# Kernel optimization log

Measured on AMD Instinct MI355X. Metric: run time of the kernel, lower is better.

## Reference

```python
import jax, jax.numpy as jnp
import numpy as np

N_NODES = 100000
N_EDGES = 1600000
N_GRAPHS = 2000
F_IN = 64
HID = 64


def setup_inputs() -> dict:
    key = jax.random.key(0)
    ks = jax.random.split(key, 8)
    h = jax.random.normal(ks[0], (N_NODES, F_IN), jnp.float32)
    edge_src = jax.random.randint(ks[1], (N_EDGES,), 0, N_NODES, jnp.int32)
    edge_dst = jax.random.randint(ks[2], (N_EDGES,), 0, N_NODES, jnp.int32)
    graph_ids = jnp.sort(jax.random.randint(ks[3], (N_NODES,), 0, N_GRAPHS, jnp.int32))
    # GraphConv weights (glorot-ish scale) and biases, 3 layers 64->64
    sc = 1.0 / np.sqrt(F_IN)
    W0 = jax.random.normal(ks[4], (F_IN, HID), jnp.float32) * sc
    W1 = jax.random.normal(ks[5], (HID, HID), jnp.float32) * sc
    W2 = jax.random.normal(ks[6], (HID, HID), jnp.float32) * sc
    b0 = jnp.zeros((HID,), jnp.float32)
    b1 = jnp.zeros((HID,), jnp.float32)
    b2 = jnp.zeros((HID,), jnp.float32)
    return dict(h=h, edge_src=edge_src, edge_dst=edge_dst, graph_ids=graph_ids,
                W0=W0, b0=b0, W1=W1, b1=b1, W2=W2, b2=b2)


def _gcn_layer(h, W, b, src, dst, out_deg_isqrt, in_deg_isqrt, apply_relu):
    # DGL GraphConv, norm='both': D_in^{-1/2} A D_out^{-1/2} h W + b
    hw = (h * out_deg_isqrt[:, None]) @ W          # weight/norm commute with sum
    m = jax.ops.segment_sum(hw[src], dst, num_segments=N_NODES)  # gather->scatter-add
    m = m * in_deg_isqrt[:, None] + b
    return jax.nn.relu(m) if apply_relu else m


def reference(h, edge_src, edge_dst, graph_ids, W0, b0, W1, b1, W2, b2):
    ones = jnp.ones((N_EDGES,), h.dtype)
    out_deg = jnp.clip(jax.ops.segment_sum(ones, edge_src, num_segments=N_NODES), 1.0, None)
    in_deg = jnp.clip(jax.ops.segment_sum(ones, edge_dst, num_segments=N_NODES), 1.0, None)
    odi = jax.lax.rsqrt(out_deg)
    idi = jax.lax.rsqrt(in_deg)
    params = [(W0, b0), (W1, b1), (W2, b2)]
    for i, (W, b) in enumerate(params):
        h = _gcn_layer(h, W, b, edge_src, edge_dst, odi, idi, apply_relu=(i < len(params) - 1))
    # self.factor = sqrt(dim) / mean(||h||) computed as python float -> detached constant
    factor = jnp.sqrt(jnp.asarray(HID, h.dtype)) / jnp.mean(jnp.linalg.norm(h, axis=1))
    factor = jax.lax.stop_gradient(factor)
    h = h * factor
    # SumPooling over batched graphs
    return jax.ops.segment_sum(h, graph_ids, num_segments=N_GRAPHS)
```

## Files before the change

kernel.cpp:

```cpp
#include <hip/hip_runtime.h>
#include <hip/hip_fp16.h>

#define N_NODES 100000
#define N_EDGES 1600000
#define N_GRAPHS 2000
#define HID 64
#define NB 391
#define CAP 5120
#define NSUP 16
#define SUPW 6400
#define CAP_S 106496
#define CH_A 2048
#define NCH_A ((N_EDGES + CH_A - 1) / CH_A)
#define BCH 4096
#define NCHB 26
#define GATHER_GRID 2048
#define GEMM_GRID 512
#define N_GROUPS (N_NODES / 4)
#define N_TILE16 (N_NODES / 16)

typedef _Float16 half8 __attribute__((ext_vector_type(8)));
typedef float f32x4 __attribute__((ext_vector_type(4)));

__global__ __launch_bounds__(256) void k_zero_i32(int* __restrict__ p, int n) {
    int i = blockIdx.x * 256 + threadIdx.x;
    if (i < n) p[i] = 0;
}

__global__ __launch_bounds__(256) void k_passA(const int* __restrict__ src, const int* __restrict__ dst,
                                               int* __restrict__ scur_dst, int* __restrict__ scur_src,
                                               unsigned* __restrict__ sup_dst,
                                               unsigned short* __restrict__ sup_src) {
    __shared__ unsigned stD[CH_A];
    __shared__ unsigned short stS[CH_A];
    __shared__ unsigned char binD[CH_A];
    __shared__ unsigned char binS[CH_A];
    __shared__ int lcntD[NSUP], lexD[NSUP], lofD[NSUP], runD[NSUP];
    __shared__ int lcntS[NSUP], lexS[NSUP], lofS[NSUP], runS[NSUP];
    int tid = threadIdx.x;
    int e0 = blockIdx.x * CH_A;
    int n = min(CH_A, N_EDGES - e0);
    if (tid < NSUP) { lcntD[tid] = 0; lcntS[tid] = 0; }
    __syncthreads();
    int sv[8], dv[8];
#pragma unroll
    for (int k = 0; k < 8; ++k) {
        int i = k * 256 + tid;
        if (i < n) { sv[k] = src[e0 + i]; dv[k] = dst[e0 + i]; }
        else dv[k] = -1;
    }
#pragma unroll
    for (int k = 0; k < 8; ++k)
        if (dv[k] >= 0) {
            atomicAdd(&lcntD[dv[k] / SUPW], 1);
            atomicAdd(&lcntS[sv[k] / SUPW], 1);
        }
    __syncthreads();
    if (tid == 0)  { int a = 0; for (int i = 0; i < NSUP; ++i) { lexD[i] = a; lofD[i] = a; a += lcntD[i]; } }
    if (tid == 64) { int a = 0; for (int i = 0; i < NSUP; ++i) { lexS[i] = a; lofS[i] = a; a += lcntS[i]; } }
    __syncthreads();
#pragma unroll
    for (int k = 0; k < 8; ++k)
        if (dv[k] >= 0) {
            int d = dv[k], s = sv[k];
            int bD = d / SUPW;
            int pD = atomicAdd(&lofD[bD], 1);
            stD[pD] = ((unsigned)(d - bD * SUPW) << 17) | (unsigned)s;
            binD[pD] = (unsigned char)bD;
            int bS = s / SUPW;
            int pS = atomicAdd(&lofS[bS], 1);
            stS[pS] = (unsigned short)(s - bS * SUPW);
            binS[pS] = (unsigned char)bS;
        }
    __syncthreads();
    if (tid < NSUP) runD[tid] = lcntD[tid] ? atomicAdd(&scur_dst[tid], lcntD[tid]) : 0;
    if (tid >= 128 && tid < 128 + NSUP) {
        int b = tid - 128;
        runS[b] = lcntS[b] ? atomicAdd(&scur_src[b], lcntS[b]) : 0;
    }
    __syncthreads();
    for (int i = tid; i < n; i += 256) {
        int b = binD[i];
        int pos = runD[b] + (i - lexD[b]);
        if (pos < CAP_S) sup_dst[(size_t)b * CAP_S + pos] = stD[i];
    }
    for (int i = tid; i < n; i += 256) {
        int b = binS[i];
        int pos = runS[b] + (i - lexS[b]);
        if (pos < CAP_S) sup_src[(size_t)b * CAP_S + pos] = stS[i];
    }
}

__global__ __launch_bounds__(256) void k_passB(const unsigned* __restrict__ sup_dst,
                                               const unsigned short* __restrict__ sup_src,
                                               const int* __restrict__ scur_dst,
                                               const int* __restrict__ scur_src,
                                               int* __restrict__ gcur_dst, int* __restrict__ gcur_src,
                                               unsigned* __restrict__ part_dst,
                                               unsigned char* __restrict__ part_src) {
    __shared__ unsigned st[BCH];
    __shared__ unsigned char bin[BCH];
    __shared__ int lcnt[25], lex[25], lof[25], run[25];
    int tid = threadIdx.x;
    int isSrc = blockIdx.x >= NSUP * NCHB;
    int bx = isSrc ? blockIdx.x - NSUP * NCHB : blockIdx.x;
    int sb = bx / NCHB, ch = bx % NCHB;
    int total = isSrc ? scur_src[sb] : scur_dst[sb];
    total = min(total, CAP_S);
    int o0 = ch * BCH;
    int n = min(BCH, total - o0);
    if (n <= 0) return;
    int bg0 = sb * 25;
    if (tid < 25) lcnt[tid] = 0;
    __syncthreads();

    if (!isSrc) {
        unsigned ev[16];
        int bb[16];
#pragma unroll
        for (int k = 0; k < 16; ++k) {
            int i = k * 256 + tid;
            if (i < n) {
                unsigned e = sup_dst[(size_t)sb * CAP_S + o0 + i];
                ev[k] = e;
                bb[k] = (int)(e >> 25);
                atomicAdd(&lcnt[bb[k]], 1);
            } else bb[k] = -1;
        }
        __syncthreads();
        if (tid == 0) { int a = 0; for (int i = 0; i < 25; ++i) { lex[i] = a; lof[i] = a; a += lcnt[i]; } }
        __syncthreads();
#pragma unroll
        for (int k = 0; k < 16; ++k)
            if (bb[k] >= 0) {
                unsigned e = ev[k];
                unsigned s = e & 0x1FFFFu;
                unsigned low = (e >> 17) & 255u;
                int p = atomicAdd(&lof[bb[k]], 1);
                st[p] = (s << 8) | low;
                bin[p] = (unsigned char)bb[k];
            }
        __syncthreads();
        if (tid < 25) run[tid] = lcnt[tid] ? atomicAdd(&gcur_dst[bg0 + tid], lcnt[tid]) : 0;
        __syncthreads();
        for (int i = tid; i < n; i += 256) {
            int b = bin[i];
            int pos = run[b] + (i - lex[b]);
            if (pos < CAP) part_dst[(size_t)(bg0 + b) * CAP + pos] = st[i];
        }
    } else {
        unsigned char* st8 = (unsigned char*)st;
        int rv[16];
        int bb[16];
#pragma unroll
        for (int k = 0; k < 16; ++k) {
            int i = k * 256 + tid;
            if (i < n) {
                int r = (int)sup_src[(size_t)sb * CAP_S + o0 + i];
                rv[k] = r;
                bb[k] = r >> 8;
                atomicAdd(&lcnt[bb[k]], 1);
            } else bb[k] = -1;
        }
        __syncthreads();
        if (tid == 0) { int a = 0; for (int i = 0; i < 25; ++i) { lex[i] = a; lof[i] = a; a += lcnt[i]; } }
        __syncthreads();
#pragma unroll
        for (int k = 0; k < 16; ++k)
            if (bb[k] >= 0) {
                int p = atomicAdd(&lof[bb[k]], 1);
                st8[p] = (unsigned char)(rv[k] & 255);
                bin[p] = (unsigned char)bb[k];
            }
        __syncthreads();
        if (tid < 25) run[tid] = lcnt[tid] ? atomicAdd(&gcur_src[bg0 + tid], lcnt[tid]) : 0;
        __syncthreads();
        for (int i = tid; i < n; i += 256) {
            int b = bin[i];
            int pos = run[b] + (i - lex[b]);
            if (pos < CAP) part_src[(size_t)(bg0 + b) * CAP + pos] = st8[i];
        }
    }
}

__global__ __launch_bounds__(256) void k_csr_count(const unsigned* __restrict__ part_dst,
                                                   const unsigned char* __restrict__ part_src,
                                                   const int* __restrict__ gcur_dst,
                                                   const int* __restrict__ gcur_src,
                                                   int* __restrict__ rowbeg, int* __restrict__ rowend,
                                                   float* __restrict__ idi, float* __restrict__ odi,
                                                   int* __restrict__ col) {
    __shared__ int cnt[256];
    __shared__ int cur[256];
    __shared__ int wsum[4];
    int tid = threadIdx.x;
    if (blockIdx.x >= NB) {
        int b = blockIdx.x - NB;
        int nE = min(gcur_src[b], CAP);
        const unsigned char* pb = part_src + (size_t)b * CAP;
        cnt[tid] = 0;
        __syncthreads();
        for (int i = tid; i < nE; i += 256) atomicAdd(&cnt[pb[i]], 1);
        __syncthreads();
        int v = b * 256 + tid;
        if (v < N_NODES) odi[v] = rsqrtf((float)max(cnt[tid], 1));
        return;
    }
    int b = blockIdx.x;
    int base = b * CAP;
    int nE = min(gcur_dst[b], CAP);
    const unsigned* pb = part_dst + (size_t)b * CAP;
    cnt[tid] = 0;
    __syncthreads();
    for (int i = tid; i < nE; i += 256) atomicAdd(&cnt[pb[i] & 255], 1);
    __syncthreads();
    int c = cnt[tid];
    int incl = c;
#pragma unroll
    for (int off = 1; off < 64; off <<= 1) {
        int t = __shfl_up(incl, off, 64);
        if ((tid & 63) >= off) incl += t;
    }
    if ((tid & 63) == 63) wsum[tid >> 6] = incl;
    __syncthreads();
    int add = 0;
    for (int w = 0; w < (tid >> 6); ++w) add += wsum[w];
    incl += add;
    int excl = incl - c;
    int v = b * 256 + tid;
    if (v < N_NODES) {
        rowbeg[v] = base + excl;
        rowend[v] = base + incl;
        idi[v] = rsqrtf((float)max(c, 1));
    }
    cur[tid] = excl;
    __syncthreads();
    for (int i = tid; i < nE; i += 256) {
        unsigned e = pb[i];
        int p = atomicAdd(&cur[e & 255], 1);
        col[base + p] = (int)(e >> 8);
    }
}

template <int F32IN>
__global__ __launch_bounds__(256) void k_gemm_mfma(const void* __restrict__ inv,
                                                   const float* __restrict__ W,
                                                   const float* __restrict__ odi,
                                                   __half* __restrict__ zs) {
    __shared__ _Float16 Wt[64 * 64];
    int tid = threadIdx.x;
    for (int i = tid; i < 4096; i += 256) {
        int k = i >> 6, j = i & 63;
        Wt[j * 64 + k] = (_Float16)W[i];
    }
    __syncthreads();

    int lane = tid & 63;
    int wid = tid >> 6;
    int lrow = lane & 15;
    int lgrp = lane >> 4;

    half8 Bf[4][2];
#pragma unroll
    for (int nt = 0; nt < 4; ++nt)
#pragma unroll
        for (int kh = 0; kh < 2; ++kh)
            Bf[nt][kh] = *(half8*)&Wt[(nt * 16 + lrow) * 64 + kh * 32 + lgrp * 8];

    for (int t = blockIdx.x * 4 + wid; t < N_TILE16; t += GEMM_GRID * 4) {
        int v0 = t * 16;
        half8 a0, a1;
        if (F32IN) {
            const float* A = (const float*)inv + (size_t)(v0 + lrow) * 64 + lgrp * 8;
            float4 f0 = *(const float4*)A;
            float4 f1 = *(const float4*)(A + 4);
            float4 g0 = *(const float4*)(A + 32);
            float4 g1 = *(const float4*)(A + 36);
            a0[0] = (_Float16)f0.x; a0[1] = (_Float16)f0.y; a0[2] = (_Float16)f0.z; a0[3] = (_Float16)f0.w;
            a0[4] = (_Float16)f1.x; a0[5] = (_Float16)f1.y; a0[6] = (_Float16)f1.z; a0[7] = (_Float16)f1.w;
            a1[0] = (_Float16)g0.x; a1[1] = (_Float16)g0.y; a1[2] = (_Float16)g0.z; a1[3] = (_Float16)g0.w;
            a1[4] = (_Float16)g1.x; a1[5] = (_Float16)g1.y; a1[6] = (_Float16)g1.z; a1[7] = (_Float16)g1.w;
        } else {
            const _Float16* A = (const _Float16*)inv + (size_t)(v0 + lrow) * 64 + lgrp * 8;
            a0 = *(const half8*)A;
            a1 = *(const half8*)(A + 32);
        }
        f32x4 acc[4];
#pragma unroll
        for (int nt = 0; nt < 4; ++nt) { acc[nt] = (f32x4)0.f; }
#pragma unroll
        for (int nt = 0; nt < 4; ++nt) {
            acc[nt] = __builtin_amdgcn_mfma_f32_16x16x32_f16(a0, Bf[nt][0], acc[nt], 0, 0, 0);
            acc[nt] = __builtin_amdgcn_mfma_f32_16x16x32_f16(a1, Bf[nt][1], acc[nt], 0, 0, 0);
        }
#pragma unroll
        for (int r = 0; r < 4; ++r) {
            int node = v0 + lgrp * 4 + r;
            float w = odi[node];
#pragma unroll
            for (int nt = 0; nt < 4; ++nt)
                zs[(size_t)node * 64 + nt * 16 + lrow] = __float2half_rn(acc[nt][r] * w);
        }
    }
}

template <int RELU, int LAST>
__global__ __launch_bounds__(256) void k_gather(const __half* __restrict__ zs, const int* __restrict__ rowbeg,
                                                const int* __restrict__ rowend, const int* __restrict__ col,
                                                const float* __restrict__ idi, const float* __restrict__ b,
                                                __half* __restrict__ xout, float* __restrict__ outF,
                                                float* __restrict__ partials) {
    __shared__ float part[4];
    int tid = threadIdx.x;
    int lane = tid & 63;
    int wid = tid >> 6;
    int half = lane >> 5;
    int fp = lane & 31;
    float2 bias2 = *(const float2*)&b[fp * 2];
    float nacc = 0.f;

    for (int g = blockIdx.x; g < N_GROUPS; g += GATHER_GRID) {
        int v = __builtin_amdgcn_readfirstlane(g * 4 + wid);
        int beg = rowbeg[v], end = rowend[v];
        float2 a0 = {0.f, 0.f}, a1 = {0.f, 0.f}, a2 = {0.f, 0.f}, a3 = {0.f, 0.f};
        int p = beg;
        for (; p + 16 <= end; p += 16) {
#pragma unroll
            for (int j = 0; j < 8; ++j) {
                int s = col[p + 2 * j + half];
                float2 f = __half22float2(*((const __half2*)(zs + (size_t)s * 64) + fp));
                if ((j & 3) == 0) { a0.x += f.x; a0.y += f.y; }
                else if ((j & 3) == 1) { a1.x += f.x; a1.y += f.y; }
                else if ((j & 3) == 2) { a2.x += f.x; a2.y += f.y; }
                else { a3.x += f.x; a3.y += f.y; }
            }
        }
        if (p + 8 <= end) {
#pragma unroll
            for (int j = 0; j < 4; ++j) {
                int s = col[p + 2 * j + half];
                float2 f = __half22float2(*((const __half2*)(zs + (size_t)s * 64) + fp));
                if (j == 0) { a0.x += f.x; a0.y += f.y; }
                else if (j == 1) { a1.x += f.x; a1.y += f.y; }
                else if (j == 2) { a2.x += f.x; a2.y += f.y; }
                else { a3.x += f.x; a3.y += f.y; }
            }
            p += 8;
        }
        if (p < end) {
#pragma unroll
            for (int j = 0; j < 4; ++j) {
                int e = p + 2 * j + half;
                int q = (e < end) ? e : (end - 1);
                int s = col[q];
                float2 f = __half22float2(*((const __half2*)(zs + (size_t)s * 64) + fp));
                float m = (e < end) ? 1.f : 0.f;
                if (j == 0) { a0.x = fmaf(f.x, m, a0.x); a0.y = fmaf(f.y, m, a0.y); }
                else if (j == 1) { a1.x = fmaf(f.x, m, a1.x); a1.y = fmaf(f.y, m, a1.y); }
                else if (j == 2) { a2.x = fmaf(f.x, m, a2.x); a2.y = fmaf(f.y, m, a2.y); }
                else { a3.x = fmaf(f.x, m, a3.x); a3.y = fmaf(f.y, m, a3.y); }
            }
        }
        float2 a;
        a.x = (a0.x + a1.x) + (a2.x + a3.x);
        a.y = (a0.y + a1.y) + (a2.y + a3.y);
        a.x += __shfl_xor(a.x, 32, 64);
        a.y += __shfl_xor(a.y, 32, 64);
        float iv = idi[v];
        float2 o;
        o.x = fmaf(a.x, iv, bias2.x);
        o.y = fmaf(a.y, iv, bias2.y);
        if (RELU) { o.x = fmaxf(o.x, 0.f); o.y = fmaxf(o.y, 0.f); }

        if (LAST) {
            if (half == 0) *(float2*)&outF[(size_t)v * 64 + fp * 2] = o;
            float s = o.x * o.x + o.y * o.y;
#pragma unroll
            for (int off = 32; off > 0; off >>= 1) s += __shfl_xor(s, off, 64);
            if (lane == 0) nacc += sqrtf(0.5f * s);
        } else {
            if (half == 0)
                *((__half2*)(xout + (size_t)v * 64) + fp) = __floats2half2_rn(o.x, o.y);
        }
    }

    if (LAST) {
        if (lane == 0) part[wid] = nacc;
        __syncthreads();
        if (tid == 0) partials[blockIdx.x] = part[0] + part[1] + part[2] + part[3];
    }
}

__global__ __launch_bounds__(256) void k_reduce_factor(const float* __restrict__ partials,
                                                       float* __restrict__ factor) {
    __shared__ float sd[256];
    int tid = threadIdx.x;
    float s = 0.f;
    for (int i = tid; i < GATHER_GRID; i += 256) s += partials[i];
    sd[tid] = s;
    __syncthreads();
    for (int off = 128; off > 0; off >>= 1) {
        if (tid < off) sd[tid] += sd[tid + off];
        __syncthreads();
    }
    if (tid == 0) factor[0] = 8.0f * (float)N_NODES / sd[0];
}

#define POOL_CHUNK 32
__global__ __launch_bounds__(256) void k_pool(const float* __restrict__ h, const int* __restrict__ gid,
                                              const float* __restrict__ factor, float* __restrict__ out) {
    int wave = (blockIdx.x * 256 + threadIdx.x) >> 6;
    int lane = threadIdx.x & 63;
    int v0 = wave * POOL_CHUNK;
    if (v0 >= N_NODES) return;
    float f = factor[0];
    int vend = min(v0 + POOL_CHUNK, N_NODES);
    int gprev = gid[v0];
    float acc = 0.f;
    for (int v = v0; v < vend; ++v) {
        int g = gid[v];
        if (g != gprev) {
            atomicAdd(&out[(size_t)gprev * 64 + lane], acc);
            acc = 0.f;
            gprev = g;
        }
        acc = fmaf(h[(size_t)v * 64 + lane], f, acc);
    }
    atomicAdd(&out[(size_t)gprev * 64 + lane], acc);
}

extern "C" void kernel_launch(void* const* d_in, const int* in_sizes, int n_in,
                              void* d_out, int out_size, void* d_ws, size_t ws_size,
                              hipStream_t stream) {
    const float* h    = (const float*)d_in[0];
    const int*   esrc = (const int*)d_in[1];
    const int*   edst = (const int*)d_in[2];
    const int*   gids = (const int*)d_in[3];
    const float* W0 = (const float*)d_in[4];
    const float* b0 = (const float*)d_in[5];
    const float* W1 = (const float*)d_in[6];
    const float* b1 = (const float*)d_in[7];
    const float* W2 = (const float*)d_in[8];
    const float* b2 = (const float*)d_in[9];
    float* out = (float*)d_out;

    char* wsp = (char*)d_ws;
    size_t off = 0;
    auto alloc = [&](size_t bytes) -> void* {
        void* p = wsp + off;
        off += (bytes + 255) & ~(size_t)255;
        return p;
    };
    int*   cursors    = (int*)alloc(814 * 4);
    float* odi        = (float*)alloc((size_t)N_NODES * 4);
    float* idi        = (float*)alloc((size_t)N_NODES * 4);
    int*   rowbeg     = (int*)alloc((size_t)N_NODES * 4);
    int*   rowend     = (int*)alloc((size_t)N_NODES * 4);
    float* partials   = (float*)alloc((size_t)GATHER_GRID * 4);
    float* factor     = (float*)alloc(4);
    int*   col        = (int*)alloc((size_t)NB * CAP * 4);
    __half* zsb       = (__half*)alloc((size_t)N_NODES * 64 * 2);
    __half* xh        = (__half*)alloc((size_t)N_NODES * 64 * 2);
    float* outF       = (float*)alloc((size_t)N_NODES * 64 * 4);
    unsigned*       sup_dst  = (unsigned*)outF;
    unsigned short* sup_src  = (unsigned short*)((char*)outF + (size_t)NSUP * CAP_S * 4);
    unsigned*       part_dst = (unsigned*)((char*)outF + (size_t)NSUP * CAP_S * 6);
    unsigned char*  part_src = (unsigned char*)((char*)outF + (size_t)NSUP * CAP_S * 6 + (size_t)NB * CAP * 4);

    int* scur_dst = cursors;
    int* scur_src = cursors + 16;
    int* gcur_dst = cursors + 32;
    int* gcur_src = cursors + 32 + NB;

    k_zero_i32<<<4, 256, 0, stream>>>(cursors, 814);
    k_zero_i32<<<(N_GRAPHS * 64 + 255) / 256, 256, 0, stream>>>((int*)out, N_GRAPHS * 64);

    k_passA<<<NCH_A, 256, 0, stream>>>(esrc, edst, scur_dst, scur_src, sup_dst, sup_src);
    k_passB<<<2 * NSUP * NCHB, 256, 0, stream>>>(sup_dst, sup_src, scur_dst, scur_src,
                                                 gcur_dst, gcur_src, part_dst, part_src);
    k_csr_count<<<2 * NB, 256, 0, stream>>>(part_dst, part_src, gcur_dst, gcur_src,
                                            rowbeg, rowend, idi, odi, col);

    k_gemm_mfma<1><<<GEMM_GRID, 256, 0, stream>>>(h, W0, odi, zsb);
    k_gather<1, 0><<<GATHER_GRID, 256, 0, stream>>>(zsb, rowbeg, rowend, col, idi, b0, xh, nullptr, nullptr);
    k_gemm_mfma<0><<<GEMM_GRID, 256, 0, stream>>>(xh, W1, odi, zsb);
    k_gather<1, 0><<<GATHER_GRID, 256, 0, stream>>>(zsb, rowbeg, rowend, col, idi, b1, xh, nullptr, nullptr);
    k_gemm_mfma<0><<<GEMM_GRID, 256, 0, stream>>>(xh, W2, odi, zsb);
    k_gather<0, 1><<<GATHER_GRID, 256, 0, stream>>>(zsb, rowbeg, rowend, col, idi, b2, nullptr, outF, partials);

    k_reduce_factor<<<1, 256, 0, stream>>>(partials, factor);
    int poolWaves  = (N_NODES + POOL_CHUNK - 1) / POOL_CHUNK;
    int poolBlocks = (poolWaves + 3) / 4;
    k_pool<<<poolBlocks, 256, 0, stream>>>(outF, gids, factor, out);
}
```

Baseline: 211.5 us.

## Preload neighbor indices per wave with shuffles, store final layer in fp16, merge zero kernels

The gather kernel now loads up to 64 column indices per node in one coalesced wave load and hands them out with shuffles, so the per-edge scalar index loads go away. Degrees above 64 fall back to a direct-load tail loop. The last layer writes fp16 into xh instead of an fp32 buffer, which halves the bytes written and later read by pooling, at the cost of some precision. The two zeroing launches are merged into one, and the scratch buffers that used to alias outF now get their own allocations.

Measured after the change: 206.5 us. -2.4%, faster.

```diff
diff --git a/kernel.cpp b/kernel.cpp
--- a/kernel.cpp
+++ b/kernel.cpp
@@ -22,9 +22,11 @@
 typedef _Float16 half8 __attribute__((ext_vector_type(8)));
 typedef float f32x4 __attribute__((ext_vector_type(4)));
 
-__global__ __launch_bounds__(256) void k_zero_i32(int* __restrict__ p, int n) {
+__global__ __launch_bounds__(256) void k_zero2(int* __restrict__ p1, int n1,
+                                               int* __restrict__ p2, int n2) {
     int i = blockIdx.x * 256 + threadIdx.x;
-    if (i < n) p[i] = 0;
+    if (i < n1) p1[i] = 0;
+    if (i < n2) p2[i] = 0;
 }
 
 __global__ __launch_bounds__(256) void k_passA(const int* __restrict__ src, const int* __restrict__ dst,
@@ -308,8 +310,7 @@
 __global__ __launch_bounds__(256) void k_gather(const __half* __restrict__ zs, const int* __restrict__ rowbeg,
                                                 const int* __restrict__ rowend, const int* __restrict__ col,
                                                 const float* __restrict__ idi, const float* __restrict__ b,
-                                                __half* __restrict__ xout, float* __restrict__ outF,
-                                                float* __restrict__ partials) {
+                                                __half* __restrict__ xout, float* __restrict__ partials) {
     __shared__ float part[4];
     int tid = threadIdx.x;
     int lane = tid & 63;
@@ -322,12 +323,15 @@
     for (int g = blockIdx.x; g < N_GROUPS; g += GATHER_GRID) {
         int v = __builtin_amdgcn_readfirstlane(g * 4 + wid);
         int beg = rowbeg[v], end = rowend[v];
+        int deg = end - beg;
+        int degS = min(deg, 64);
+        int c = col[beg + min(lane, max(degS - 1, 0))];
         float2 a0 = {0.f, 0.f}, a1 = {0.f, 0.f}, a2 = {0.f, 0.f}, a3 = {0.f, 0.f};
-        int p = beg;
-        for (; p + 16 <= end; p += 16) {
+        int m = 0;
+        for (; (m + 8) * 2 <= degS; m += 8) {
 #pragma unroll
             for (int j = 0; j < 8; ++j) {
-                int s = col[p + 2 * j + half];
+                int s = __shfl(c, 2 * (m + j) + half, 64);
                 float2 f = __half22float2(*((const __half2*)(zs + (size_t)s * 64) + fp));
                 if ((j & 3) == 0) { a0.x += f.x; a0.y += f.y; }
                 else if ((j & 3) == 1) { a1.x += f.x; a1.y += f.y; }
@@ -335,30 +339,43 @@
                 else { a3.x += f.x; a3.y += f.y; }
             }
         }
-        if (p + 8 <= end) {
+        if ((m + 4) * 2 <= degS) {
 #pragma unroll
             for (int j = 0; j < 4; ++j) {
-                int s = col[p + 2 * j + half];
+                int s = __shfl(c, 2 * (m + j) + half, 64);
                 float2 f = __half22float2(*((const __half2*)(zs + (size_t)s * 64) + fp));
                 if (j == 0) { a0.x += f.x; a0.y += f.y; }
                 else if (j == 1) { a1.x += f.x; a1.y += f.y; }
                 else if (j == 2) { a2.x += f.x; a2.y += f.y; }
                 else { a3.x += f.x; a3.y += f.y; }
             }
-            p += 8;
-        }
-        if (p < end) {
+            m += 4;
+        }
+        if (m * 2 < degS) {
 #pragma unroll
             for (int j = 0; j < 4; ++j) {
-                int e = p + 2 * j + half;
-                int q = (e < end) ? e : (end - 1);
-                int s = col[q];
+                int e = 2 * (m + j) + half;
+                int ee = (e < degS) ? e : (degS - 1);
+                int s = __shfl(c, ee, 64);
                 float2 f = __half22float2(*((const __half2*)(zs + (size_t)s * 64) + fp));
-                float m = (e < end) ? 1.f : 0.f;
-                if (j == 0) { a0.x = fmaf(f.x, m, a0.x); a0.y = fmaf(f.y, m, a0.y); }
-                else if (j == 1) { a1.x = fmaf(f.x, m, a1.x); a1.y = fmaf(f.y, m, a1.y); }
-                else if (j == 2) { a2.x = fmaf(f.x, m, a2.x); a2.y = fmaf(f.y, m, a2.y); }
-                else { a3.x = fmaf(f.x, m, a3.x); a3.y = fmaf(f.y, m, a3.y); }
+                float msk = (e < degS) ? 1.f : 0.f;
+                if (j == 0) { a0.x = fmaf(f.x, msk, a0.x); a0.y = fmaf(f.y, msk, a0.y); }
+                else if (j == 1) { a1.x = fmaf(f.x, msk, a1.x); a1.y = fmaf(f.y, msk, a1.y); }
+                else if (j == 2) { a2.x = fmaf(f.x, msk, a2.x); a2.y = fmaf(f.y, msk, a2.y); }
+                else { a3.x = fmaf(f.x, msk, a3.x); a3.y = fmaf(f.y, msk, a3.y); }
+            }
+        }
+        if (deg > 64) {
+            for (int p = beg + 64; p < end; p += 8) {
+#pragma unroll
+                for (int j = 0; j < 4; ++j) {
+                    int e = p + 2 * j + half;
+                    int q = (e < end) ? e : (end - 1);
+                    int s = col[q];
+                    float2 f = __half22float2(*((const __half2*)(zs + (size_t)s * 64) + fp));
+                    float msk = (e < end) ? 1.f : 0.f;
+                    a0.x = fmaf(f.x, msk, a0.x); a0.y = fmaf(f.y, msk, a0.y);
+                }
             }
         }
         float2 a;
@@ -372,15 +389,14 @@
         o.y = fmaf(a.y, iv, bias2.y);
         if (RELU) { o.x = fmaxf(o.x, 0.f); o.y = fmaxf(o.y, 0.f); }
 
+        if (half == 0)
+            *((__half2*)(xout + (size_t)v * 64) + fp) = __floats2half2_rn(o.x, o.y);
+
         if (LAST) {
-            if (half == 0) *(float2*)&outF[(size_t)v * 64 + fp * 2] = o;
             float s = o.x * o.x + o.y * o.y;
 #pragma unroll
             for (int off = 32; off > 0; off >>= 1) s += __shfl_xor(s, off, 64);
             if (lane == 0) nacc += sqrtf(0.5f * s);
-        } else {
-            if (half == 0)
-                *((__half2*)(xout + (size_t)v * 64) + fp) = __floats2half2_rn(o.x, o.y);
         }
     }
 
@@ -407,7 +423,7 @@
 }
 
 #define POOL_CHUNK 32
-__global__ __launch_bounds__(256) void k_pool(const float* __restrict__ h, const int* __restrict__ gid,
+__global__ __launch_bounds__(256) void k_pool(const __half* __restrict__ h, const int* __restrict__ gid,
                                               const float* __restrict__ factor, float* __restrict__ out) {
     int wave = (blockIdx.x * 256 + threadIdx.x) >> 6;
     int lane = threadIdx.x & 63;
@@ -424,7 +440,7 @@
             acc = 0.f;
             gprev = g;
         }
-        acc = fmaf(h[(size_t)v * 64 + lane], f, acc);
+        acc = fmaf(__half2float(h[(size_t)v * 64 + lane]), f, acc);
     }
     atomicAdd(&out[(size_t)gprev * 64 + lane], acc);
 }
@@ -461,19 +477,17 @@
     int*   col        = (int*)alloc((size_t)NB * CAP * 4);
     __half* zsb       = (__half*)alloc((size_t)N_NODES * 64 * 2);
     __half* xh        = (__half*)alloc((size_t)N_NODES * 64 * 2);
-    float* outF       = (float*)alloc((size_t)N_NODES * 64 * 4);
-    unsigned*       sup_dst  = (unsigned*)outF;
-    unsigned short* sup_src  = (unsigned short*)((char*)outF + (size_t)NSUP * CAP_S * 4);
-    unsigned*       part_dst = (unsigned*)((char*)outF + (size_t)NSUP * CAP_S * 6);
-    unsigned char*  part_src = (unsigned char*)((char*)outF + (size_t)NSUP * CAP_S * 6 + (size_t)NB * CAP * 4);
+    unsigned*       sup_dst  = (unsigned*)alloc((size_t)NSUP * CAP_S * 4);
+    unsigned short* sup_src  = (unsigned short*)alloc((size_t)NSUP * CAP_S * 2);
+    unsigned*       part_dst = (unsigned*)alloc((size_t)NB * CAP * 4);
+    unsigned char*  part_src = (unsigned char*)alloc((size_t)NB * CAP);
 
     int* scur_dst = cursors;
     int* scur_src = cursors + 16;
     int* gcur_dst = cursors + 32;
     int* gcur_src = cursors + 32 + NB;
 
-    k_zero_i32<<<4, 256, 0, stream>>>(cursors, 814);
-    k_zero_i32<<<(N_GRAPHS * 64 + 255) / 256, 256, 0, stream>>>((int*)out, N_GRAPHS * 64);
+    k_zero2<<<(N_GRAPHS * 64 + 255) / 256, 256, 0, stream>>>(cursors, 814, (int*)out, N_GRAPHS * 64);
 
     k_passA<<<NCH_A, 256, 0, stream>>>(esrc, edst, scur_dst, scur_src, sup_dst, sup_src);
     k_passB<<<2 * NSUP * NCHB, 256, 0, stream>>>(sup_dst, sup_src, scur_dst, scur_src,
@@ -482,14 +496,14 @@
                                             rowbeg, rowend, idi, odi, col);
 
     k_gemm_mfma<1><<<GEMM_GRID, 256, 0, stream>>>(h, W0, odi, zsb);
-    k_gather<1, 0><<<GATHER_GRID, 256, 0, stream>>>(zsb, rowbeg, rowend, col, idi, b0, xh, nullptr, nullptr);
+    k_gather<1, 0><<<GATHER_GRID, 256, 0, stream>>>(zsb, rowbeg, rowend, col, idi, b0, xh, nullptr);
     k_gemm_mfma<0><<<GEMM_GRID, 256, 0, stream>>>(xh, W1, odi, zsb);
-    k_gather<1, 0><<<GATHER_GRID, 256, 0, stream>>>(zsb, rowbeg, rowend, col, idi, b1, xh, nullptr, nullptr);
+    k_gather<1, 0><<<GATHER_GRID, 256, 0, stream>>>(zsb, rowbeg, rowend, col, idi, b1, xh, nullptr);
     k_gemm_mfma<0><<<GEMM_GRID, 256, 0, stream>>>(xh, W2, odi, zsb);
-    k_gather<0, 1><<<GATHER_GRID, 256, 0, stream>>>(zsb, rowbeg, rowend, col, idi, b2, nullptr, outF, partials);
+    k_gather<0, 1><<<GATHER_GRID, 256, 0, stream>>>(zsb, rowbeg, rowend, col, idi, b2, xh, partials);
 
     k_reduce_factor<<<1, 256, 0, stream>>>(partials, factor);
     int poolWaves  = (N_NODES + POOL_CHUNK - 1) / POOL_CHUNK;
     int poolBlocks = (poolWaves + 3) / 4;
-    k_pool<<<poolBlocks, 256, 0, stream>>>(outF, gids, factor, out);
-}
+    k_pool<<<poolBlocks, 256, 0, stream>>>(xh, gids, factor, out);
+}
```
